# Performance work log

Hardware: AMD Instinct MI355X
Metric: run time of the kernel (lower is better)

Reference implementation:

```python
import jax, jax.numpy as jnp
import numpy as np

D_MODEL = 1024
N_HEADS = 16
HEAD_DIM = D_MODEL // N_HEADS
ROPE_BASE = 10000.0
RMS_EPS = 1e-5


def setup_inputs() -> dict:
    key = jax.random.key(0)
    k1, k2, k3 = jax.random.split(key, 3)
    B, T = 2, 2048
    x = jax.random.normal(k1, (B, T, D_MODEL), dtype=jnp.float32)
    norm_w = jnp.ones((D_MODEL,), dtype=jnp.float32)
    w_qkv = jax.random.normal(k2, (3 * D_MODEL, D_MODEL), dtype=jnp.float32) * (D_MODEL ** -0.5)
    w_out = jax.random.normal(k3, (D_MODEL, D_MODEL), dtype=jnp.float32) * (D_MODEL ** -0.5)
    return {"x": x, "norm_w": norm_w, "w_qkv": w_qkv, "w_out": w_out}


def _rope_cos_sin(T, dtype):
    inv_freq = 1.0 / (ROPE_BASE ** (jnp.arange(0, HEAD_DIM, 2, dtype=jnp.float32) / HEAD_DIM))
    t = jnp.arange(T, dtype=jnp.float32)
    freqs = t[:, None] * inv_freq[None, :]            # [T, HEAD_DIM//2]
    emb = jnp.concatenate([freqs, freqs], axis=-1)    # [T, HEAD_DIM]
    return jnp.cos(emb).astype(dtype), jnp.sin(emb).astype(dtype)


def _rotate_half(x):
    x1, x2 = jnp.split(x, 2, axis=-1)
    return jnp.concatenate([-x2, x1], axis=-1)


def reference(x, norm_w, w_qkv, w_out):
    B, T, _ = x.shape
    residual = x
    # RMSNorm
    rms = jax.lax.rsqrt(jnp.mean(x * x, axis=-1, keepdims=True) + RMS_EPS)
    xn = x * rms * norm_w
    # QKV projection (torch Linear: x @ W.T)
    qkv = xn @ w_qkv.T                                  # [B, T, 3*D]
    qkv = qkv.reshape(B, T, 3, N_HEADS, HEAD_DIM)
    q, k, v = qkv[:, :, 0], qkv[:, :, 1], qkv[:, :, 2]  # [B, T, H, hd]
    # RoPE on q, k
    cos, sin = _rope_cos_sin(T, q.dtype)                # [T, hd]
    cos = cos[None, :, None, :]
    sin = sin[None, :, None, :]
    q = q * cos + _rotate_half(q) * sin
    k = k * cos + _rotate_half(k) * sin
    # Bidirectional SDPA: [B, H, T, hd]
    qh = q.transpose(0, 2, 1, 3)
    kh = k.transpose(0, 2, 1, 3)
    vh = v.transpose(0, 2, 1, 3)
    scale = HEAD_DIM ** -0.5
    scores = jnp.einsum('bhqd,bhkd->bhqk', qh, kh) * scale
    attn = jax.nn.softmax(scores, axis=-1)
    out = jnp.einsum('bhqk,bhkd->bhqd', attn, vh)       # [B, H, T, hd]
    out = out.transpose(0, 2, 1, 3).reshape(B, T, D_MODEL)
    out = out @ w_out.T
    return residual + out
```

## Files before the change

kernel.cpp:

```cpp
#include <hip/hip_runtime.h>
#include <hip/hip_bf16.h>
#include <math.h>


typedef __bf16 bf16;
typedef __bf16 bf16x8 __attribute__((ext_vector_type(8)));
typedef __bf16 bf16x4 __attribute__((ext_vector_type(4)));
typedef float  f32x4  __attribute__((ext_vector_type(4)));
typedef unsigned u32x4 __attribute__((ext_vector_type(4)));

#define GLOAD16(g, l) __builtin_amdgcn_global_load_lds( \
    (const __attribute__((address_space(1))) void*)(g),  \
    (__attribute__((address_space(3))) void*)(l), 16, 0, 0)

__device__ __forceinline__ unsigned pk2(float a, float b) {
  unsigned short lo = __builtin_bit_cast(unsigned short, (bf16)a);
  unsigned short hi = __builtin_bit_cast(unsigned short, (bf16)b);
  return (unsigned)lo | ((unsigned)hi << 16);
}

__global__ __launch_bounds__(256) void k_cvt(const float* __restrict__ src,
    bf16* __restrict__ dst, int n) {
  int i = (blockIdx.x * 256 + threadIdx.x) * 8;
  if (i >= n) return;
  float4 a = *(const float4*)(src + i);
  float4 b = *(const float4*)(src + i + 4);
  bf16x8 o;
  o[0] = (bf16)a.x; o[1] = (bf16)a.y; o[2] = (bf16)a.z; o[3] = (bf16)a.w;
  o[4] = (bf16)b.x; o[5] = (bf16)b.y; o[6] = (bf16)b.z; o[7] = (bf16)b.w;
  *(bf16x8*)(dst + i) = o;
}

__global__ __launch_bounds__(256) void k_rmsnorm(const float* __restrict__ x,
    const float* __restrict__ w, bf16* __restrict__ xn) {
  const int row = blockIdx.x, tid = threadIdx.x;
  float4 v = *(const float4*)(x + (size_t)row * 1024 + tid * 4);
  float ss = v.x * v.x + v.y * v.y + v.z * v.z + v.w * v.w;
  for (int m = 32; m >= 1; m >>= 1) ss += __shfl_xor(ss, m);
  __shared__ float red[4];
  if ((tid & 63) == 0) red[tid >> 6] = ss;
  __syncthreads();
  float ms = (red[0] + red[1] + red[2] + red[3]) * (1.f / 1024.f);
  float r = rsqrtf(ms + 1e-5f);
  float4 wv = *(const float4*)(w + tid * 4);
  bf16x4 o;
  o[0] = (bf16)(v.x * r * wv.x); o[1] = (bf16)(v.y * r * wv.y);
  o[2] = (bf16)(v.z * r * wv.z); o[3] = (bf16)(v.w * r * wv.w);
  *(bf16x4*)(xn + (size_t)row * 1024 + tid * 4) = o;
}

template<int RESID>
__global__ __launch_bounds__(256, 2) void k_gemm_bt(const bf16* __restrict__ A,
    const bf16* __restrict__ B, const float* __restrict__ R, void* __restrict__ Cv,
    int M, int N, int K, int lda) {
  const int tid = threadIdx.x;
  const int lane = tid & 63, L15 = lane & 15, quad = lane >> 4;
  const int wave = tid >> 6, wr = wave >> 1, wc = wave & 1;
  const int n0 = blockIdx.x * 128, m0 = blockIdx.y * 128;
  __shared__ __align__(16) bf16 smem[17408];
  bf16* sA = smem; bf16* sB = smem + 8192;
  f32x4 acc[4][4];
  const f32x4 z = {0.f, 0.f, 0.f, 0.f};
  for (int i = 0; i < 4; i++) for (int j = 0; j < 4; j++) acc[i][j] = z;

  for (int k0 = 0; k0 < K; k0 += 64) {
    const bf16* Ab = A + (size_t)m0 * lda + k0;
    const bf16* Bb = B + (size_t)n0 * K + k0;
    for (int p = 0; p < 4; p++) {
      int s = p * 256 + tid, r = s >> 3, c8 = (s & 7) ^ (r & 7);
      GLOAD16(Ab + (size_t)r * lda + c8 * 8, sA + s * 8);
      GLOAD16(Bb + (size_t)r * K + c8 * 8, sB + s * 8);
    }
    __syncthreads();
    for (int kk = 0; kk < 2; kk++) {
      bf16x8 af[4], bfv[4];
      for (int i = 0; i < 4; i++) {
        int ra = wr * 64 + i * 16 + L15;
        af[i] = *(const bf16x8*)(sA + ra * 64 + (((kk * 4 + quad) ^ (ra & 7)) * 8));
        int rb = wc * 64 + i * 16 + L15;
        bfv[i] = *(const bf16x8*)(sB + rb * 64 + (((kk * 4 + quad) ^ (rb & 7)) * 8));
      }
      for (int mt = 0; mt < 4; mt++)
        for (int nt = 0; nt < 4; nt++)
          acc[mt][nt] = __builtin_amdgcn_mfma_f32_16x16x32_bf16(af[mt], bfv[nt], acc[mt][nt], 0, 0, 0);
    }
    __syncthreads();
  }
  bf16* sC = smem;
  for (int mt = 0; mt < 4; mt++) for (int nt = 0; nt < 4; nt++) {
    int r = wr * 64 + mt * 16 + quad * 4, c = wc * 64 + nt * 16 + L15;
    f32x4 v = acc[mt][nt];
    for (int g = 0; g < 4; g++) sC[(r + g) * 136 + c] = (bf16)v[g];
  }
  __syncthreads();
  const int rr = tid >> 1, sg = (tid & 1) * 64;
  const size_t row = (size_t)m0 + rr;
  const bf16* src = sC + rr * 136 + sg;
  if (RESID) {
    float* Cf = (float*)Cv;
    const float* rs = R + row * N + n0 + sg;
    float* dst = Cf + row * N + n0 + sg;
    for (int i = 0; i < 16; i++) {
      bf16x4 u = *(const bf16x4*)(src + i * 4);
      float4 rv = *(const float4*)(rs + i * 4);
      float4 o;
      o.x = (float)u[0] + rv.x; o.y = (float)u[1] + rv.y;
      o.z = (float)u[2] + rv.z; o.w = (float)u[3] + rv.w;
      *(float4*)(dst + i * 4) = o;
    }
  } else {
    bf16* Cb = (bf16*)Cv;
    bf16* dst = Cb + row * N + n0 + sg;
    for (int i = 0; i < 8; i++)
      *(bf16x8*)(dst + i * 8) = *(const bf16x8*)(src + i * 8);
  }
}

__global__ __launch_bounds__(256) void k_rope(bf16* __restrict__ qkv,
    bf16* __restrict__ vt) {
  const int blk = blockIdx.x;
  const int tt = blk & 31, h = (blk >> 5) & 15, b = blk >> 9;
  const int tid = threadIdx.x;
  const int bh = b * 16 + h;
  {
    const int tl = tid >> 2, dp = (tid & 3) * 8;
    const int tg = tt * 64 + tl;
    bf16* base = qkv + (size_t)(b * 2048 + tg) * 3072 + h * 64;
    bf16x8 qlo = *(const bf16x8*)(base + dp);
    bf16x8 qhi = *(const bf16x8*)(base + dp + 32);
    bf16x8 klo = *(const bf16x8*)(base + 1024 + dp);
    bf16x8 khi = *(const bf16x8*)(base + 1024 + dp + 32);
    bf16x8 oql, oqh, okl, okh;
    for (int j = 0; j < 8; j++) {
      float invf = exp2f(-0.41524101186f * (float)(dp + j));
      float th = (float)tg * invf;
      float sn, cs;
      sincosf(th, &sn, &cs);
      float a0 = (float)qlo[j], a1 = (float)qhi[j];
      float b0 = (float)klo[j], b1 = (float)khi[j];
      oql[j] = (bf16)(a0 * cs - a1 * sn);
      oqh[j] = (bf16)(a1 * cs + a0 * sn);
      okl[j] = (bf16)(b0 * cs - b1 * sn);
      okh[j] = (bf16)(b1 * cs + b0 * sn);
    }
    *(bf16x8*)(base + dp) = oql; *(bf16x8*)(base + dp + 32) = oqh;
    *(bf16x8*)(base + 1024 + dp) = okl; *(bf16x8*)(base + 1024 + dp + 32) = okh;
  }
  __shared__ __align__(16) bf16 sT[64 * 72];
  for (int p = 0; p < 2; p++) {
    int s = p * 256 + tid, tl = s >> 3, c = s & 7;
    const bf16* vsrc = qkv + (size_t)(b * 2048 + tt * 64 + tl) * 3072 + 2048 + h * 64 + c * 8;
    *(bf16x8*)(sT + tl * 72 + c * 8) = *(const bf16x8*)vsrc;
  }
  __syncthreads();
  for (int p = 0; p < 2; p++) {
    int s = p * 256 + tid, d = s >> 3, tc = s & 7;
    bf16x8 v;
    for (int j = 0; j < 8; j++) v[j] = sT[(tc * 8 + j) * 72 + d];
    *(bf16x8*)(vt + (size_t)bh * 131072 + (size_t)d * 2048 + tt * 64 + tc * 8) = v;
  }
}

__global__ __launch_bounds__(256, 2) void k_attn(bf16* __restrict__ qkv,
    const bf16* __restrict__ vt) {
  const int tid = threadIdx.x;
  const int lane = tid & 63, L15 = lane & 15, quad = lane >> 4;
  const int wave = tid >> 6;
  const int bh = blockIdx.y, b = bh >> 4, h = bh & 15;
  const int q0 = blockIdx.x * 128;
  const bf16* Q  = qkv + (size_t)b * 2048 * 3072 + h * 64;
  const bf16* Kg = qkv + (size_t)b * 2048 * 3072 + 1024 + h * 64;
  const bf16* Vg = vt + (size_t)bh * 131072;
  __shared__ __align__(16) bf16 smem[32768];

  bf16x8 qf[2][2];
  for (int qt = 0; qt < 2; qt++) for (int kk = 0; kk < 2; kk++) {
    int rq = q0 + wave * 32 + qt * 16 + L15;
    qf[qt][kk] = *(const bf16x8*)(Q + (size_t)rq * 3072 + kk * 32 + quad * 8);
  }
  f32x4 o[4][2];
  const f32x4 z = {0.f, 0.f, 0.f, 0.f};
  for (int i = 0; i < 4; i++) for (int j = 0; j < 2; j++) o[i][j] = z;
  f32x4 o5[2] = {z, z};
  const bf16 one = (bf16)1.0f;
  const bf16x8 ones8 = {one, one, one, one, one, one, one, one};
  float mrun[2] = {-1e30f, -1e30f};
  const float c2l = 0.125f * 1.44269504089f;

  auto STAGE = [&](int kv0, int base) {
    const bf16* Kb = Kg + (size_t)kv0 * 3072;
    bf16* sKb = smem + base;
    bf16* sVb = smem + base + 8192;
    for (int p = 0; p < 4; p++) {
      int s = p * 256 + tid, r = s >> 3, c8 = (s & 7) ^ (r & 7);
      GLOAD16(Kb + (size_t)r * 3072 + c8 * 8, sKb + s * 8);
    }
    for (int p = 0; p < 4; p++) {
      int s = p * 256 + tid, r = s >> 4, cl = s & 15;
      int c8 = (cl & 8) | ((cl ^ (r & 7)) & 7);
      GLOAD16(Vg + (size_t)r * 2048 + kv0 + c8 * 8, sVb + s * 8);
    }
  };

  STAGE(0, 0);
  for (int t = 0; t < 16; ++t) {
    const int cur = (t & 1) << 14;
    if (t < 15) {
      STAGE((t + 1) << 7, cur ^ 16384);
      asm volatile("s_waitcnt vmcnt(8)" ::: "memory");
    } else {
      asm volatile("s_waitcnt vmcnt(0)" ::: "memory");
    }
    __builtin_amdgcn_s_barrier();
    __builtin_amdgcn_sched_barrier(0);
    const bf16* sK = smem + cur;
    const bf16* sV = smem + cur + 8192;

    f32x4 st[8][2];
#pragma unroll
    for (int i = 0; i < 8; i++) for (int j = 0; j < 2; j++) st[i][j] = z;
#pragma unroll
    for (int kk = 0; kk < 2; kk++) {
      bf16x8 kf[8];
#pragma unroll
      for (int kvt = 0; kvt < 8; kvt++) {
        int rk = kvt * 16 + L15;
        kf[kvt] = *(const bf16x8*)(sK + rk * 64 + (((kk * 4 + quad) ^ (rk & 7)) * 8));
      }
#pragma unroll
      for (int kvt = 0; kvt < 8; kvt++)
        for (int qt = 0; qt < 2; qt++)
          st[kvt][qt] = __builtin_amdgcn_mfma_f32_16x16x32_bf16(kf[kvt], qf[qt][kk], st[kvt][qt], 0, 0, 0);
    }
    unsigned pA[2][8], pB[2][8];
#pragma unroll
    for (int qt = 0; qt < 2; qt++) {
      float m = st[0][qt][0];
#pragma unroll
      for (int kvt = 0; kvt < 8; kvt++)
        for (int g = 0; g < 4; g++) m = fmaxf(m, st[kvt][qt][g]);
      m = fmaxf(m, __shfl_xor(m, 16));
      m = fmaxf(m, __shfl_xor(m, 32));
      if (__any(m > mrun[qt] + 8.f)) {
        float mnew = fmaxf(mrun[qt], m);
        float alpha = __builtin_amdgcn_exp2f((mrun[qt] - mnew) * c2l);
#pragma unroll
        for (int dt = 0; dt < 4; dt++) o[dt][qt] *= alpha;
        o5[qt] *= alpha;
        mrun[qt] = mnew;
      }
      float mc = mrun[qt] * c2l;
#pragma unroll
      for (int kvt = 0; kvt < 8; kvt++) {
        float p0 = __builtin_amdgcn_exp2f(st[kvt][qt][0] * c2l - mc);
        float p1 = __builtin_amdgcn_exp2f(st[kvt][qt][1] * c2l - mc);
        float p2 = __builtin_amdgcn_exp2f(st[kvt][qt][2] * c2l - mc);
        float p3 = __builtin_amdgcn_exp2f(st[kvt][qt][3] * c2l - mc);
        pA[qt][kvt] = pk2(p0, p1);
        pB[qt][kvt] = pk2(p2, p3);
      }
    }
#pragma unroll
    for (int kc = 0; kc < 4; kc++) {
      bf16x8 vf[4];
#pragma unroll
      for (int dt = 0; dt < 4; dt++) {
        int rd = dt * 16 + L15;
        int c = kc * 4 + quad;
        int cs = (c & 8) | ((c ^ (rd & 7)) & 7);
        vf[dt] = *(const bf16x8*)(sV + rd * 128 + cs * 8);
      }
#pragma unroll
      for (int qt = 0; qt < 2; qt++) {
        auto rA = __builtin_amdgcn_permlane32_swap(pA[qt][2 * kc], pA[qt][2 * kc + 1], false, false);
        auto tAC = __builtin_amdgcn_permlane16_swap(rA[0], rA[1], false, false);
        auto rB = __builtin_amdgcn_permlane32_swap(pB[qt][2 * kc], pB[qt][2 * kc + 1], false, false);
        auto tBD = __builtin_amdgcn_permlane16_swap(rB[0], rB[1], false, false);
        u32x4 pw;
        pw[0] = tAC[0]; pw[1] = tBD[0]; pw[2] = tAC[1]; pw[3] = tBD[1];
        bf16x8 pf = __builtin_bit_cast(bf16x8, pw);
#pragma unroll
        for (int dt = 0; dt < 4; dt++)
          o[dt][qt] = __builtin_amdgcn_mfma_f32_16x16x32_bf16(vf[dt], pf, o[dt][qt], 0, 0, 0);
        o5[qt] = __builtin_amdgcn_mfma_f32_16x16x32_bf16(ones8, pf, o5[qt], 0, 0, 0);
      }
    }
    asm volatile("s_waitcnt lgkmcnt(0)" ::: "memory");
    __builtin_amdgcn_sched_barrier(0);
    __builtin_amdgcn_s_barrier();
  }
  float invl[2] = {1.f / o5[0][0], 1.f / o5[1][0]};
  bf16* sO = smem;
  for (int dt = 0; dt < 4; dt++) for (int qt = 0; qt < 2; qt++) {
    f32x4 v = o[dt][qt] * invl[qt];
    int ql = wave * 32 + qt * 16 + L15;
    uint2 w2; w2.x = pk2(v[0], v[1]); w2.y = pk2(v[2], v[3]);
    *(uint2*)(sO + ql * 72 + dt * 16 + quad * 4) = w2;
  }
  __syncthreads();
  const int rr = tid >> 1, sg = (tid & 1) * 32;
  const bf16* src = sO + rr * 72 + sg;
  bf16* dst = qkv + (size_t)(b * 2048 + q0 + rr) * 3072 + h * 64 + sg;
  for (int i = 0; i < 4; i++)
    *(bf16x8*)(dst + i * 8) = *(const bf16x8*)(src + i * 8);
}

extern "C" void kernel_launch(void* const* d_in, const int* in_sizes, int n_in,
                              void* d_out, int out_size, void* d_ws, size_t ws_size,
                              hipStream_t stream) {
  (void)in_sizes; (void)n_in; (void)out_size;
  const float* x     = (const float*)d_in[0];
  const float* normw = (const float*)d_in[1];
  const float* wqkv  = (const float*)d_in[2];
  const float* wout  = (const float*)d_in[3];
  float* out = (float*)d_out;
  bf16* ws  = (bf16*)d_ws;
  const size_t NQKV = (size_t)4096 * 3072, NXN = (size_t)4096 * 1024;
  const size_t NWQ = (size_t)3072 * 1024, NWO = (size_t)1024 * 1024;
  const size_t need = (NQKV + NXN + NWQ + NWO) * sizeof(bf16);
  if (ws_size < need) return;
  bf16* qkv    = ws;
  bf16* xn     = qkv + NQKV;
  bf16* vtp    = xn;
  bf16* wqkvb  = xn + NXN;
  bf16* woutb  = wqkvb + NWQ;
  k_cvt<<<(int)(NWQ / 8 / 256), 256, 0, stream>>>(wqkv, wqkvb, (int)NWQ);
  k_cvt<<<(int)(NWO / 8 / 256), 256, 0, stream>>>(wout, woutb, (int)NWO);
  k_rmsnorm<<<4096, 256, 0, stream>>>(x, normw, xn);
  k_gemm_bt<0><<<dim3(24, 32), 256, 0, stream>>>(xn, wqkvb, nullptr, qkv, 4096, 3072, 1024, 1024);
  k_rope<<<1024, 256, 0, stream>>>(qkv, vtp);
  k_attn<<<dim3(16, 32), 256, 0, stream>>>(qkv, vtp);
  k_gemm_bt<1><<<dim3(8, 32), 256, 0, stream>>>(qkv, woutb, x, out, 4096, 1024, 1024, 3072);
}
```

Before: 211.8 us.

## Split attention block across eight waves with one 16-row Q tile each

The attention kernel now launches 512 threads per block, so each of the eight waves handles 16 query rows instead of 32. K/V staging is shared by more threads, so each thread issues half as many async loads, and the wait count is adjusted to match. Per-wave register use drops, and the launch bounds ask for more resident waves to hide latency. s_setprio is also raised around the MFMA bursts. In exchange, each K/V fragment read from LDS now feeds only one MFMA per wave, so LDS traffic per unit of compute doubles.

Result: no change. 208.6 us (-1.5%).

```diff
diff --git a/kernel.cpp b/kernel.cpp
--- a/kernel.cpp
+++ b/kernel.cpp
@@ -161,7 +161,7 @@
   }
 }
 
-__global__ __launch_bounds__(256, 2) void k_attn(bf16* __restrict__ qkv,
+__global__ __launch_bounds__(512, 4) void k_attn(bf16* __restrict__ qkv,
     const bf16* __restrict__ vt) {
   const int tid = threadIdx.x;
   const int lane = tid & 63, L15 = lane & 15, quad = lane >> 4;
@@ -173,30 +173,31 @@
   const bf16* Vg = vt + (size_t)bh * 131072;
   __shared__ __align__(16) bf16 smem[32768];
 
-  bf16x8 qf[2][2];
-  for (int qt = 0; qt < 2; qt++) for (int kk = 0; kk < 2; kk++) {
-    int rq = q0 + wave * 32 + qt * 16 + L15;
-    qf[qt][kk] = *(const bf16x8*)(Q + (size_t)rq * 3072 + kk * 32 + quad * 8);
-  }
-  f32x4 o[4][2];
+  bf16x8 qf[2];
+  {
+    int rq = q0 + wave * 16 + L15;
+    for (int kk = 0; kk < 2; kk++)
+      qf[kk] = *(const bf16x8*)(Q + (size_t)rq * 3072 + kk * 32 + quad * 8);
+  }
+  f32x4 o[4];
   const f32x4 z = {0.f, 0.f, 0.f, 0.f};
-  for (int i = 0; i < 4; i++) for (int j = 0; j < 2; j++) o[i][j] = z;
-  f32x4 o5[2] = {z, z};
+  for (int i = 0; i < 4; i++) o[i] = z;
+  f32x4 o5 = z;
   const bf16 one = (bf16)1.0f;
   const bf16x8 ones8 = {one, one, one, one, one, one, one, one};
-  float mrun[2] = {-1e30f, -1e30f};
+  float mrun = -1e30f;
   const float c2l = 0.125f * 1.44269504089f;
 
   auto STAGE = [&](int kv0, int base) {
     const bf16* Kb = Kg + (size_t)kv0 * 3072;
     bf16* sKb = smem + base;
     bf16* sVb = smem + base + 8192;
-    for (int p = 0; p < 4; p++) {
-      int s = p * 256 + tid, r = s >> 3, c8 = (s & 7) ^ (r & 7);
+    for (int p = 0; p < 2; p++) {
+      int s = p * 512 + tid, r = s >> 3, c8 = (s & 7) ^ (r & 7);
       GLOAD16(Kb + (size_t)r * 3072 + c8 * 8, sKb + s * 8);
     }
-    for (int p = 0; p < 4; p++) {
-      int s = p * 256 + tid, r = s >> 4, cl = s & 15;
+    for (int p = 0; p < 2; p++) {
+      int s = p * 512 + tid, r = s >> 4, cl = s & 15;
       int c8 = (cl & 8) | ((cl ^ (r & 7)) & 7);
       GLOAD16(Vg + (size_t)r * 2048 + kv0 + c8 * 8, sVb + s * 8);
     }
@@ -207,7 +208,7 @@
     const int cur = (t & 1) << 14;
     if (t < 15) {
       STAGE((t + 1) << 7, cur ^ 16384);
-      asm volatile("s_waitcnt vmcnt(8)" ::: "memory");
+      asm volatile("s_waitcnt vmcnt(4)" ::: "memory");
     } else {
       asm volatile("s_waitcnt vmcnt(0)" ::: "memory");
     }
@@ -216,9 +217,9 @@
     const bf16* sK = smem + cur;
     const bf16* sV = smem + cur + 8192;
 
-    f32x4 st[8][2];
-#pragma unroll
-    for (int i = 0; i < 8; i++) for (int j = 0; j < 2; j++) st[i][j] = z;
+    f32x4 st[8];
+#pragma unroll
+    for (int i = 0; i < 8; i++) st[i] = z;
 #pragma unroll
     for (int kk = 0; kk < 2; kk++) {
       bf16x8 kf[8];
@@ -227,37 +228,37 @@
         int rk = kvt * 16 + L15;
         kf[kvt] = *(const bf16x8*)(sK + rk * 64 + (((kk * 4 + quad) ^ (rk & 7)) * 8));
       }
+      __builtin_amdgcn_s_setprio(1);
 #pragma unroll
       for (int kvt = 0; kvt < 8; kvt++)
-        for (int qt = 0; qt < 2; qt++)
-          st[kvt][qt] = __builtin_amdgcn_mfma_f32_16x16x32_bf16(kf[kvt], qf[qt][kk], st[kvt][qt], 0, 0, 0);
-    }
-    unsigned pA[2][8], pB[2][8];
-#pragma unroll
-    for (int qt = 0; qt < 2; qt++) {
-      float m = st[0][qt][0];
+        st[kvt] = __builtin_amdgcn_mfma_f32_16x16x32_bf16(kf[kvt], qf[kk], st[kvt], 0, 0, 0);
+      __builtin_amdgcn_s_setprio(0);
+    }
+    unsigned pA[8], pB[8];
+    {
+      float m = st[0][0];
 #pragma unroll
       for (int kvt = 0; kvt < 8; kvt++)
-        for (int g = 0; g < 4; g++) m = fmaxf(m, st[kvt][qt][g]);
+        for (int g = 0; g < 4; g++) m = fmaxf(m, st[kvt][g]);
       m = fmaxf(m, __shfl_xor(m, 16));
       m = fmaxf(m, __shfl_xor(m, 32));
-      if (__any(m > mrun[qt] + 8.f)) {
-        float mnew = fmaxf(mrun[qt], m);
-        float alpha = __builtin_amdgcn_exp2f((mrun[qt] - mnew) * c2l);
-#pragma unroll
-        for (int dt = 0; dt < 4; dt++) o[dt][qt] *= alpha;
-        o5[qt] *= alpha;
-        mrun[qt] = mnew;
-      }
-      float mc = mrun[qt] * c2l;
+      if (__any(m > mrun + 8.f)) {
+        float mnew = fmaxf(mrun, m);
+        float alpha = __builtin_amdgcn_exp2f((mrun - mnew) * c2l);
+#pragma unroll
+        for (int dt = 0; dt < 4; dt++) o[dt] *= alpha;
+        o5 *= alpha;
+        mrun = mnew;
+      }
+      float mc = mrun * c2l;
 #pragma unroll
       for (int kvt = 0; kvt < 8; kvt++) {
-        float p0 = __builtin_amdgcn_exp2f(st[kvt][qt][0] * c2l - mc);
-        float p1 = __builtin_amdgcn_exp2f(st[kvt][qt][1] * c2l - mc);
-        float p2 = __builtin_amdgcn_exp2f(st[kvt][qt][2] * c2l - mc);
-        float p3 = __builtin_amdgcn_exp2f(st[kvt][qt][3] * c2l - mc);
-        pA[qt][kvt] = pk2(p0, p1);
-        pB[qt][kvt] = pk2(p2, p3);
+        float p0 = __builtin_amdgcn_exp2f(st[kvt][0] * c2l - mc);
+        float p1 = __builtin_amdgcn_exp2f(st[kvt][1] * c2l - mc);
+        float p2 = __builtin_amdgcn_exp2f(st[kvt][2] * c2l - mc);
+        float p3 = __builtin_amdgcn_exp2f(st[kvt][3] * c2l - mc);
+        pA[kvt] = pk2(p0, p1);
+        pB[kvt] = pk2(p2, p3);
       }
     }
 #pragma unroll
@@ -270,38 +271,37 @@
         int cs = (c & 8) | ((c ^ (rd & 7)) & 7);
         vf[dt] = *(const bf16x8*)(sV + rd * 128 + cs * 8);
       }
-#pragma unroll
-      for (int qt = 0; qt < 2; qt++) {
-        auto rA = __builtin_amdgcn_permlane32_swap(pA[qt][2 * kc], pA[qt][2 * kc + 1], false, false);
-        auto tAC = __builtin_amdgcn_permlane16_swap(rA[0], rA[1], false, false);
-        auto rB = __builtin_amdgcn_permlane32_swap(pB[qt][2 * kc], pB[qt][2 * kc + 1], false, false);
-        auto tBD = __builtin_amdgcn_permlane16_swap(rB[0], rB[1], false, false);
-        u32x4 pw;
-        pw[0] = tAC[0]; pw[1] = tBD[0]; pw[2] = tAC[1]; pw[3] = tBD[1];
-        bf16x8 pf = __builtin_bit_cast(bf16x8, pw);
-#pragma unroll
-        for (int dt = 0; dt < 4; dt++)
-          o[dt][qt] = __builtin_amdgcn_mfma_f32_16x16x32_bf16(vf[dt], pf, o[dt][qt], 0, 0, 0);
-        o5[qt] = __builtin_amdgcn_mfma_f32_16x16x32_bf16(ones8, pf, o5[qt], 0, 0, 0);
-      }
+      auto rA = __builtin_amdgcn_permlane32_swap(pA[2 * kc], pA[2 * kc + 1], false, false);
+      auto tAC = __builtin_amdgcn_permlane16_swap(rA[0], rA[1], false, false);
+      auto rB = __builtin_amdgcn_permlane32_swap(pB[2 * kc], pB[2 * kc + 1], false, false);
+      auto tBD = __builtin_amdgcn_permlane16_swap(rB[0], rB[1], false, false);
+      u32x4 pw;
+      pw[0] = tAC[0]; pw[1] = tBD[0]; pw[2] = tAC[1]; pw[3] = tBD[1];
+      bf16x8 pf = __builtin_bit_cast(bf16x8, pw);
+      __builtin_amdgcn_s_setprio(1);
+#pragma unroll
+      for (int dt = 0; dt < 4; dt++)
+        o[dt] = __builtin_amdgcn_mfma_f32_16x16x32_bf16(vf[dt], pf, o[dt], 0, 0, 0);
+      o5 = __builtin_amdgcn_mfma_f32_16x16x32_bf16(ones8, pf, o5, 0, 0, 0);
+      __builtin_amdgcn_s_setprio(0);
     }
     asm volatile("s_waitcnt lgkmcnt(0)" ::: "memory");
     __builtin_amdgcn_sched_barrier(0);
     __builtin_amdgcn_s_barrier();
   }
-  float invl[2] = {1.f / o5[0][0], 1.f / o5[1][0]};
+  float invl = 1.f / o5[0];
   bf16* sO = smem;
-  for (int dt = 0; dt < 4; dt++) for (int qt = 0; qt < 2; qt++) {
-    f32x4 v = o[dt][qt] * invl[qt];
-    int ql = wave * 32 + qt * 16 + L15;
+  for (int dt = 0; dt < 4; dt++) {
+    f32x4 v = o[dt] * invl;
+    int ql = wave * 16 + L15;
     uint2 w2; w2.x = pk2(v[0], v[1]); w2.y = pk2(v[2], v[3]);
     *(uint2*)(sO + ql * 72 + dt * 16 + quad * 4) = w2;
   }
   __syncthreads();
-  const int rr = tid >> 1, sg = (tid & 1) * 32;
+  const int rr = tid >> 2, sg = (tid & 3) * 16;
   const bf16* src = sO + rr * 72 + sg;
   bf16* dst = qkv + (size_t)(b * 2048 + q0 + rr) * 3072 + h * 64 + sg;
-  for (int i = 0; i < 4; i++)
+  for (int i = 0; i < 2; i++)
     *(bf16x8*)(dst + i * 8) = *(const bf16x8*)(src + i * 8);
 }
 
@@ -329,6 +329,6 @@
   k_rmsnorm<<<4096, 256, 0, stream>>>(x, normw, xn);
   k_gemm_bt<0><<<dim3(24, 32), 256, 0, stream>>>(xn, wqkvb, nullptr, qkv, 4096, 3072, 1024, 1024);
   k_rope<<<1024, 256, 0, stream>>>(qkv, vtp);
-  k_attn<<<dim3(16, 32), 256, 0, stream>>>(qkv, vtp);
+  k_attn<<<dim3(16, 32), 512, 0, stream>>>(qkv, vtp);
   k_gemm_bt<1><<<dim3(8, 32), 256, 0, stream>>>(qkv, woutb, x, out, 4096, 1024, 1024, 3072);
 }
```
